# Kernel optimization log

Hardware: AMD Instinct MI355X
Metric: run time of the kernel (lower is better)

Reference implementation:

```python
import jax, jax.numpy as jnp
import numpy as np

B, N_EX, N_KC, D_E, D_C, D_H = 32, 1024, 128, 64, 64, 64


def setup_inputs() -> dict:
    key = jax.random.key(0)
    ks = jax.random.split(key, 20)
    return {
        "h": jax.random.normal(ks[0], (B, N_KC, D_H), jnp.float32),
        "ex": jax.random.uniform(ks[1], (B, N_EX), jnp.float32),
        "su": jax.random.uniform(ks[2], (B,), jnp.float32),
        "ex_graph": jax.random.uniform(ks[3], (N_EX, N_KC), jnp.float32),
        "kc_gamma": jax.random.normal(ks[4], (N_KC, N_KC), jnp.float32),
        "W_ex": jax.random.normal(ks[5], (D_E, 2 * N_EX), jnp.float32) * 0.02,
        "W_kc": jax.random.normal(ks[6], (D_C, N_KC), jnp.float32) * 0.05,
        "tgru_wih": jax.random.normal(ks[7], (3 * D_H, D_E), jnp.float32) * 0.05,
        "tgru_whh": jax.random.normal(ks[8], (3 * D_H, D_H), jnp.float32) * 0.05,
        "tgru_bih": jax.random.normal(ks[9], (3 * D_H,), jnp.float32) * 0.05,
        "tgru_bhh": jax.random.normal(ks[10], (3 * D_H,), jnp.float32) * 0.05,
        "fpart_w": jax.random.normal(ks[11], (D_H, D_C + D_H), jnp.float32) * 0.05,
        "fpart_b": jax.random.normal(ks[12], (D_H,), jnp.float32) * 0.05,
        "ulin_w": jax.random.normal(ks[13], (D_H, D_H), jnp.float32) * 0.05,
        "ulin_b": jax.random.normal(ks[14], (D_H,), jnp.float32) * 0.05,
        "ugru_wih": jax.random.normal(ks[15], (3 * D_H, D_H), jnp.float32) * 0.05,
        "ugru_whh": jax.random.normal(ks[16], (3 * D_H, D_H), jnp.float32) * 0.05,
        "ugru_bih": jax.random.normal(ks[17], (3 * D_H,), jnp.float32) * 0.05,
        "ugru_bhh": jax.random.normal(ks[18], (3 * D_H,), jnp.float32) * 0.05,
    }


def _gru_cell(x, h, wih, whh, bih, bhh):
    # torch.nn.GRUCell: gates in order r, z, n
    gi = x @ wih.T + bih
    gh = h @ whh.T + bhh
    ir, iz, inn = jnp.split(gi, 3, axis=-1)
    hr, hz, hn = jnp.split(gh, 3, axis=-1)
    r = jax.nn.sigmoid(ir + hr)
    z = jax.nn.sigmoid(iz + hz)
    n = jnp.tanh(inn + r * hn)
    return (1.0 - z) * n + z * h


def reference(h, ex, su, ex_graph, kc_gamma, W_ex, W_kc,
              tgru_wih, tgru_whh, tgru_bih, tgru_bhh,
              fpart_w, fpart_b, ulin_w, ulin_b,
              ugru_wih, ugru_whh, ugru_bih, ugru_bhh):
    bsz, n_kc, d_h = h.shape
    kc_graph = jax.nn.sigmoid(kc_gamma)  # (n_kc, n_kc)

    # exercise embedding from [ex*su, ex*(1-su)]
    x_id = jnp.concatenate([ex * su[:, None], ex * (1.0 - su)[:, None]], axis=-1)  # (B, 2*n_ex)
    x = x_id @ W_ex.T  # (B, d_e)

    kci = ex @ ex_graph  # (B, n_kc)
    kci_flat = kci.reshape(bsz * n_kc, 1)

    # temporal GRU update, gated by kci
    x_rep = jnp.broadcast_to(x[:, None, :], (bsz, n_kc, x.shape[-1])).reshape(bsz * n_kc, -1)
    h_flat = h.reshape(bsz * n_kc, d_h)
    th = _gru_cell(x_rep, h_flat, tgru_wih, tgru_whh, tgru_bih, tgru_bhh)
    new_h = (1.0 - kci_flat) * h_flat + kci_flat * th  # (B*n_kc, d_h)

    delta_h = (new_h - h_flat).reshape(bsz, n_kc, d_h)

    # kc_embeddings(eye(n_kc)) == W_kc.T : (n_kc, d_c)
    e = W_kc.T
    # fpart(concat([delta_h_i, e_j])) split into the two weight blocks
    W_dh = fpart_w[:, :d_h]   # acts on delta_h
    W_e = fpart_w[:, d_h:]    # acts on e
    dpart = delta_h @ W_dh.T                      # (B, n_kc_i, d_h)
    epart = e @ W_e.T + fpart_b                   # (n_kc_j, d_h)
    pre = dpart[:, :, None, :] + epart[None, None, :, :]  # (B, i, j, d_h)
    partij = jax.nn.relu(pre)
    partij = partij * kc_graph[None, :, :, None] * kci[:, :, None, None]
    partj = jnp.sum(partij, axis=1)               # (B, n_kc_j, d_h)

    outj = jax.nn.relu(partj @ ulin_w.T + ulin_b).reshape(bsz * n_kc, d_h)
    kcj = (kci @ kc_graph).reshape(bsz * n_kc, 1)

    uh = _gru_cell(outj, new_h, ugru_wih, ugru_whh, ugru_bih, ugru_bhh)
    h_out = (1.0 - kcj) * new_h + kcj * uh
    return h_out.reshape(bsz, n_kc, d_h)
```

## Files before the change

### kernel.cpp

```cpp
#include <hip/hip_runtime.h>
#include <math.h>

#define NB  32
#define NKC 128
#define DH  64
#define NEX 1024
#define G3  192

#define XOFF    0
#define KCIOFF  2048
#define KCGOFF  6144
#define EPOFF   22528
#define NHOFF   30720
#define DPOFF   292864

__device__ __forceinline__ float sigf(float x) { return 1.0f / (1.0f + expf(-x)); }

__global__ __launch_bounds__(256) void k1_prep(
    const float* __restrict__ ex, const float* __restrict__ su,
    const float* __restrict__ ex_graph, const float* __restrict__ kc_gamma,
    const float* __restrict__ W_ex, const float* __restrict__ W_kc,
    const float* __restrict__ fpart_w, const float* __restrict__ fpart_b,
    float* __restrict__ ws)
{
    int t = threadIdx.x, wave = t >> 6, lane = t & 63;
    int blk = blockIdx.x;
    __shared__ float kred[256];
    __shared__ float fwT[64 * 65];
    __shared__ float wkS[64 * 33];

    if (blk < 256) {
        int b = blk >> 3;
        int dbase = (blk & 7) * 8;
        float sub = su[b];
        const float* exb = ex + (size_t)b * NEX;
        float er[16];
        #pragma unroll
        for (int i = 0; i < 16; ++i) er[i] = exb[lane + i * 64];
        #pragma unroll
        for (int p = 0; p < 2; ++p) {
            int d = dbase + wave * 2 + p;
            const float* wr = W_ex + (size_t)d * (2 * NEX);
            float a1 = 0.f, a2 = 0.f;
            #pragma unroll
            for (int i = 0; i < 16; ++i) {
                int k = lane + i * 64;
                a1 = fmaf(er[i], wr[k], a1);
                a2 = fmaf(er[i], wr[NEX + k], a2);
            }
            float v = sub * a1 + (1.0f - sub) * a2;
            #pragma unroll
            for (int off = 32; off; off >>= 1) v += __shfl_down(v, off, 64);
            if (lane == 0) ws[XOFF + b * DH + d] = v;
        }
    } else if (blk < 384) {
        int q = blk - 256;
        int b = q >> 2, i0 = (q & 3) * 32;
        int i = t & 31, ks = t >> 5;
        const float* exb = ex + (size_t)b * NEX;
        const float* eg = ex_graph + i0 + i;
        int kb = ks * 128;
        float a = 0.f;
        for (int k = 0; k < 128; ++k)
            a = fmaf(exb[kb + k], eg[(size_t)(kb + k) * NKC], a);
        kred[t] = a;
        __syncthreads();
        if (t < 32) {
            float s = 0.f;
            #pragma unroll
            for (int r = 0; r < 8; ++r) s += kred[r * 32 + t];
            ws[KCIOFF + b * NKC + i0 + t] = s;
        }
    } else if (blk < 400) {
        int q = blk - 384;
        #pragma unroll
        for (int r = 0; r < 4; ++r) {
            int idx = q * 1024 + r * 256 + t;
            ws[KCGOFF + idx] = sigf(kc_gamma[idx]);
        }
    } else {
        int eb = blk - 400;
        for (int idx = t; idx < 4096; idx += 256) {
            int d = idx >> 6, c = idx & 63;
            fwT[c * 65 + d] = fpart_w[d * 128 + 64 + c];
        }
        for (int idx = t; idx < 2048; idx += 256) {
            int c = idx >> 5, jl = idx & 31;
            wkS[c * 33 + jl] = W_kc[(size_t)c * NKC + eb * 32 + jl];
        }
        __syncthreads();
        float fb = fpart_b[lane];
        #pragma unroll
        for (int q2 = 0; q2 < 8; ++q2) {
            int jl = wave + 4 * q2;
            float a = fb;
            for (int c = 0; c < 64; ++c)
                a = fmaf(wkS[c * 33 + jl], fwT[c * 65 + lane], a);
            ws[EPOFF + (eb * 32 + jl) * DH + lane] = a;
        }
    }
}

__global__ __launch_bounds__(256) void k2_tgru(
    const float* __restrict__ h, const float* __restrict__ tgru_wih,
    const float* __restrict__ tgru_whh, const float* __restrict__ tgru_bih,
    const float* __restrict__ tgru_bhh, const float* __restrict__ fpart_w,
    float* __restrict__ ws)
{
    int t = threadIdx.x, wave = t >> 6, lane = t & 63;
    int b = blockIdx.x >> 2;
    int i0 = (blockIdx.x & 3) * 32;
    __shared__ float whhT[32 * 193];
    __shared__ float wihT[32 * 193];
    __shared__ float ht[32 * DH];
    __shared__ float dlt[32 * DH];
    __shared__ float xs[DH];
    __shared__ float bih3[G3];
    __shared__ float bhh3[G3];
    __shared__ float kcis[32];

    const float* hb = h + (size_t)(b * NKC + i0) * DH;
    for (int idx = t; idx < 32 * DH; idx += 256) ht[idx] = hb[idx];
    if (t < DH) xs[t] = ws[XOFF + b * DH + t];
    if (t < G3) { bih3[t] = tgru_bih[t]; bhh3[t] = tgru_bhh[t]; }
    if (t < 32) kcis[t] = ws[KCIOFF + b * NKC + i0 + t];
    __syncthreads();

    float gir = bih3[lane], giz = bih3[64 + lane], gin = bih3[128 + lane];
    float ar[8], az[8], an[8];
    #pragma unroll
    for (int m = 0; m < 8; ++m) {
        ar[m] = bhh3[lane]; az[m] = bhh3[64 + lane]; an[m] = bhh3[128 + lane];
    }

    for (int ch = 0; ch < 2; ++ch) {
        __syncthreads();
        for (int idx = t; idx < G3 * 32; idx += 256) {
            int row = idx >> 5, kk = idx & 31;
            whhT[kk * 193 + row] = tgru_whh[row * DH + ch * 32 + kk];
            wihT[kk * 193 + row] = tgru_wih[row * DH + ch * 32 + kk];
        }
        __syncthreads();
        for (int kk = 0; kk < 32; ++kk) {
            float wr = whhT[kk * 193 + lane];
            float wz = whhT[kk * 193 + 64 + lane];
            float wn = whhT[kk * 193 + 128 + lane];
            float xk = xs[ch * 32 + kk];
            gir = fmaf(wihT[kk * 193 + lane], xk, gir);
            giz = fmaf(wihT[kk * 193 + 64 + lane], xk, giz);
            gin = fmaf(wihT[kk * 193 + 128 + lane], xk, gin);
            int k = ch * 32 + kk;
            #pragma unroll
            for (int m = 0; m < 8; ++m) {
                float hk = ht[(wave * 8 + m) * DH + k];
                ar[m] = fmaf(wr, hk, ar[m]);
                az[m] = fmaf(wz, hk, az[m]);
                an[m] = fmaf(wn, hk, an[m]);
            }
        }
    }
    #pragma unroll
    for (int m = 0; m < 8; ++m) {
        int il = wave * 8 + m;
        float hval = ht[il * DH + lane];
        float r = sigf(gir + ar[m]);
        float z = sigf(giz + az[m]);
        float n = tanhf(gin + r * an[m]);
        float th = (1.0f - z) * n + z * hval;
        float kv = kcis[il];
        float nh = (1.0f - kv) * hval + kv * th;
        ws[NHOFF + (size_t)(b * NKC + i0 + il) * DH + lane] = nh;
        dlt[il * DH + lane] = kv * (th - hval);
    }
    __syncthreads();
    for (int idx = t; idx < 4096; idx += 256) {
        int d = idx >> 6, k = idx & 63;
        whhT[k * 65 + d] = fpart_w[d * 128 + k];
    }
    __syncthreads();
    float acc[8];
    #pragma unroll
    for (int m = 0; m < 8; ++m) acc[m] = 0.f;
    for (int k = 0; k < 64; ++k) {
        float w = whhT[k * 65 + lane];
        #pragma unroll
        for (int m = 0; m < 8; ++m)
            acc[m] = fmaf(dlt[(wave * 8 + m) * DH + k], w, acc[m]);
    }
    #pragma unroll
    for (int m = 0; m < 8; ++m)
        ws[DPOFF + (size_t)(b * NKC + i0 + wave * 8 + m) * DH + lane] = acc[m];
}

__global__ __launch_bounds__(256) void k3_update(
    const float* __restrict__ ulin_w, const float* __restrict__ ulin_b,
    const float* __restrict__ ugru_wih, const float* __restrict__ ugru_whh,
    const float* __restrict__ ugru_bih, const float* __restrict__ ugru_bhh,
    float* __restrict__ ws, float* __restrict__ out)
{
    int t = threadIdx.x, wave = t >> 6, lane = t & 63;
    int b = blockIdx.x >> 3;
    int j0 = (blockIdx.x & 7) * 16;

    __shared__ float scratch[12352];
    __shared__ float pjS[16 * DH];
    __shared__ float outjS[16 * DH];
    __shared__ float newhS[16 * DH];
    __shared__ float kcis[NKC];
    __shared__ float kcjS[16];
    __shared__ float bihS[G3];
    __shared__ float bhhS[G3];

    float* dpartS = scratch;
    float* wjS    = scratch + 8192;
    float* epS    = scratch + 10240;

    const float* dp = ws + DPOFF + (size_t)b * NKC * DH;
    for (int idx = t; idx < NKC * DH; idx += 256) dpartS[idx] = dp[idx];
    if (t < NKC) kcis[t] = ws[KCIOFF + b * NKC + t];
    for (int idx = t; idx < 16 * DH; idx += 256) {
        epS[idx]   = ws[EPOFF + j0 * DH + idx];
        newhS[idx] = ws[NHOFF + (size_t)(b * NKC + j0) * DH + idx];
    }
    if (t < G3) { bihS[t] = ugru_bih[t]; bhhS[t] = ugru_bhh[t]; }
    __syncthreads();
    for (int idx = t; idx < 2048; idx += 256) {
        int i = idx >> 4, jl = idx & 15;
        wjS[idx] = kcis[i] * ws[KCGOFF + i * NKC + j0 + jl];
    }
    __syncthreads();
    if (t < 16) {
        float s = 0.f;
        for (int i = 0; i < NKC; ++i) s += wjS[i * 16 + t];
        kcjS[t] = s;
    }
    float ep[4], pa[4];
    #pragma unroll
    for (int q = 0; q < 4; ++q) { ep[q] = epS[(wave + 4 * q) * DH + lane]; pa[q] = 0.f; }
    for (int i = 0; i < NKC; ++i) {
        float dv = dpartS[i * DH + lane];
        #pragma unroll
        for (int q = 0; q < 4; ++q) {
            float pre = fmaxf(dv + ep[q], 0.f);
            pa[q] = fmaf(pre, wjS[i * 16 + wave + 4 * q], pa[q]);
        }
    }
    #pragma unroll
    for (int q = 0; q < 4; ++q) pjS[(wave + 4 * q) * DH + lane] = pa[q];
    __syncthreads();
    float* ulT = scratch;
    for (int idx = t; idx < 4096; idx += 256) {
        int d2 = idx >> 6, k = idx & 63;
        ulT[k * 65 + d2] = ulin_w[d2 * DH + k];
    }
    float ulb = ulin_b[lane];
    __syncthreads();
    #pragma unroll
    for (int q = 0; q < 4; ++q) {
        int jl = wave + 4 * q;
        float a = ulb;
        for (int k = 0; k < DH; ++k) a = fmaf(pjS[jl * DH + k], ulT[k * 65 + lane], a);
        outjS[jl * DH + lane] = fmaxf(a, 0.f);
    }
    float* wihT = scratch;
    float* whhT = scratch + 6176;
    float gir[4], giz[4], gin[4], ghr[4], ghz[4], ghn[4];
    #pragma unroll
    for (int q = 0; q < 4; ++q) { gir[q] = giz[q] = gin[q] = ghr[q] = ghz[q] = ghn[q] = 0.f; }
    for (int ch = 0; ch < 2; ++ch) {
        __syncthreads();
        for (int idx = t; idx < G3 * 32; idx += 256) {
            int row = idx >> 5, kk = idx & 31;
            wihT[kk * 193 + row] = ugru_wih[row * DH + ch * 32 + kk];
            whhT[kk * 193 + row] = ugru_whh[row * DH + ch * 32 + kk];
        }
        __syncthreads();
        for (int kk = 0; kk < 32; ++kk) {
            float wir = wihT[kk * 193 + lane];
            float wiz = wihT[kk * 193 + 64 + lane];
            float win = wihT[kk * 193 + 128 + lane];
            float wwr = whhT[kk * 193 + lane];
            float wwz = whhT[kk * 193 + 64 + lane];
            float wwn = whhT[kk * 193 + 128 + lane];
            int k = ch * 32 + kk;
            #pragma unroll
            for (int q = 0; q < 4; ++q) {
                int jl = wave + 4 * q;
                float ov = outjS[jl * DH + k];
                float nv = newhS[jl * DH + k];
                gir[q] = fmaf(wir, ov, gir[q]);
                giz[q] = fmaf(wiz, ov, giz[q]);
                gin[q] = fmaf(win, ov, gin[q]);
                ghr[q] = fmaf(wwr, nv, ghr[q]);
                ghz[q] = fmaf(wwz, nv, ghz[q]);
                ghn[q] = fmaf(wwn, nv, ghn[q]);
            }
        }
    }
    #pragma unroll
    for (int q = 0; q < 4; ++q) {
        int jl = wave + 4 * q;
        float r = sigf(gir[q] + bihS[lane] + ghr[q] + bhhS[lane]);
        float z = sigf(giz[q] + bihS[64 + lane] + ghz[q] + bhhS[64 + lane]);
        float n = tanhf(gin[q] + bihS[128 + lane] + r * (ghn[q] + bhhS[128 + lane]));
        float nh = newhS[jl * DH + lane];
        float uh = (1.0f - z) * n + z * nh;
        float kj = kcjS[jl];
        out[(size_t)(b * NKC + j0 + jl) * DH + lane] = (1.0f - kj) * nh + kj * uh;
    }
}

extern "C" void kernel_launch(void* const* d_in, const int* in_sizes, int n_in,
                              void* d_out, int out_size, void* d_ws, size_t ws_size,
                              hipStream_t stream) {
    const float* h        = (const float*)d_in[0];
    const float* ex       = (const float*)d_in[1];
    const float* su       = (const float*)d_in[2];
    const float* ex_graph = (const float*)d_in[3];
    const float* kc_gamma = (const float*)d_in[4];
    const float* W_ex     = (const float*)d_in[5];
    const float* W_kc     = (const float*)d_in[6];
    const float* tgru_wih = (const float*)d_in[7];
    const float* tgru_whh = (const float*)d_in[8];
    const float* tgru_bih = (const float*)d_in[9];
    const float* tgru_bhh = (const float*)d_in[10];
    const float* fpart_w  = (const float*)d_in[11];
    const float* fpart_b  = (const float*)d_in[12];
    const float* ulin_w   = (const float*)d_in[13];
    const float* ulin_b   = (const float*)d_in[14];
    const float* ugru_wih = (const float*)d_in[15];
    const float* ugru_whh = (const float*)d_in[16];
    const float* ugru_bih = (const float*)d_in[17];
    const float* ugru_bhh = (const float*)d_in[18];
    float* ws  = (float*)d_ws;
    float* out = (float*)d_out;

    hipLaunchKernelGGL(k1_prep, dim3(404), dim3(256), 0, stream,
                       ex, su, ex_graph, kc_gamma, W_ex, W_kc,
                       fpart_w, fpart_b, ws);
    hipLaunchKernelGGL(k2_tgru, dim3(128), dim3(256), 0, stream,
                       h, tgru_wih, tgru_whh, tgru_bih, tgru_bhh, fpart_w, ws);
    hipLaunchKernelGGL(k3_update, dim3(256), dim3(256), 0, stream,
                       ulin_w, ulin_b, ugru_wih, ugru_whh, ugru_bih, ugru_bhh,
                       ws, out);
}
```

Measured before the change: 150.2 us.

## Fuse prep kernel into GRU and update kernels, dropping one launch

Removes the separate prep kernel. The GRU kernel now computes the exercise projection x and kci itself from a shared-memory copy of ex, and its first four blocks also compute epart. The update kernel computes sigmoid(kc_gamma) inline instead of reading a precomputed table. This saves a kernel launch and the workspace round-trip, in exchange for redundant W_ex reads across the four blocks per batch (each now does all 64 dims) and longer serial work per block with only 128 blocks.

```diff
diff --git a/kernel.cpp b/kernel.cpp
--- a/kernel.cpp
+++ b/kernel.cpp
@@ -7,109 +7,27 @@
 #define NEX 1024
 #define G3  192
 
-#define XOFF    0
-#define KCIOFF  2048
-#define KCGOFF  6144
-#define EPOFF   22528
-#define NHOFF   30720
-#define DPOFF   292864
+#define KCIOFF  0
+#define EPOFF   4096
+#define NHOFF   12288
+#define DPOFF   274432
 
 __device__ __forceinline__ float sigf(float x) { return 1.0f / (1.0f + expf(-x)); }
 
-__global__ __launch_bounds__(256) void k1_prep(
-    const float* __restrict__ ex, const float* __restrict__ su,
-    const float* __restrict__ ex_graph, const float* __restrict__ kc_gamma,
+__global__ __launch_bounds__(256) void kA_tgru(
+    const float* __restrict__ h, const float* __restrict__ ex,
+    const float* __restrict__ su, const float* __restrict__ ex_graph,
     const float* __restrict__ W_ex, const float* __restrict__ W_kc,
+    const float* __restrict__ tgru_wih, const float* __restrict__ tgru_whh,
+    const float* __restrict__ tgru_bih, const float* __restrict__ tgru_bhh,
     const float* __restrict__ fpart_w, const float* __restrict__ fpart_b,
-    float* __restrict__ ws)
-{
-    int t = threadIdx.x, wave = t >> 6, lane = t & 63;
-    int blk = blockIdx.x;
-    __shared__ float kred[256];
-    __shared__ float fwT[64 * 65];
-    __shared__ float wkS[64 * 33];
-
-    if (blk < 256) {
-        int b = blk >> 3;
-        int dbase = (blk & 7) * 8;
-        float sub = su[b];
-        const float* exb = ex + (size_t)b * NEX;
-        float er[16];
-        #pragma unroll
-        for (int i = 0; i < 16; ++i) er[i] = exb[lane + i * 64];
-        #pragma unroll
-        for (int p = 0; p < 2; ++p) {
-            int d = dbase + wave * 2 + p;
-            const float* wr = W_ex + (size_t)d * (2 * NEX);
-            float a1 = 0.f, a2 = 0.f;
-            #pragma unroll
-            for (int i = 0; i < 16; ++i) {
-                int k = lane + i * 64;
-                a1 = fmaf(er[i], wr[k], a1);
-                a2 = fmaf(er[i], wr[NEX + k], a2);
-            }
-            float v = sub * a1 + (1.0f - sub) * a2;
-            #pragma unroll
-            for (int off = 32; off; off >>= 1) v += __shfl_down(v, off, 64);
-            if (lane == 0) ws[XOFF + b * DH + d] = v;
-        }
-    } else if (blk < 384) {
-        int q = blk - 256;
-        int b = q >> 2, i0 = (q & 3) * 32;
-        int i = t & 31, ks = t >> 5;
-        const float* exb = ex + (size_t)b * NEX;
-        const float* eg = ex_graph + i0 + i;
-        int kb = ks * 128;
-        float a = 0.f;
-        for (int k = 0; k < 128; ++k)
-            a = fmaf(exb[kb + k], eg[(size_t)(kb + k) * NKC], a);
-        kred[t] = a;
-        __syncthreads();
-        if (t < 32) {
-            float s = 0.f;
-            #pragma unroll
-            for (int r = 0; r < 8; ++r) s += kred[r * 32 + t];
-            ws[KCIOFF + b * NKC + i0 + t] = s;
-        }
-    } else if (blk < 400) {
-        int q = blk - 384;
-        #pragma unroll
-        for (int r = 0; r < 4; ++r) {
-            int idx = q * 1024 + r * 256 + t;
-            ws[KCGOFF + idx] = sigf(kc_gamma[idx]);
-        }
-    } else {
-        int eb = blk - 400;
-        for (int idx = t; idx < 4096; idx += 256) {
-            int d = idx >> 6, c = idx & 63;
-            fwT[c * 65 + d] = fpart_w[d * 128 + 64 + c];
-        }
-        for (int idx = t; idx < 2048; idx += 256) {
-            int c = idx >> 5, jl = idx & 31;
-            wkS[c * 33 + jl] = W_kc[(size_t)c * NKC + eb * 32 + jl];
-        }
-        __syncthreads();
-        float fb = fpart_b[lane];
-        #pragma unroll
-        for (int q2 = 0; q2 < 8; ++q2) {
-            int jl = wave + 4 * q2;
-            float a = fb;
-            for (int c = 0; c < 64; ++c)
-                a = fmaf(wkS[c * 33 + jl], fwT[c * 65 + lane], a);
-            ws[EPOFF + (eb * 32 + jl) * DH + lane] = a;
-        }
-    }
-}
-
-__global__ __launch_bounds__(256) void k2_tgru(
-    const float* __restrict__ h, const float* __restrict__ tgru_wih,
-    const float* __restrict__ tgru_whh, const float* __restrict__ tgru_bih,
-    const float* __restrict__ tgru_bhh, const float* __restrict__ fpart_w,
     float* __restrict__ ws)
 {
     int t = threadIdx.x, wave = t >> 6, lane = t & 63;
     int b = blockIdx.x >> 2;
     int i0 = (blockIdx.x & 3) * 32;
+
+    __shared__ float exs[NEX];
     __shared__ float whhT[32 * 193];
     __shared__ float wihT[32 * 193];
     __shared__ float ht[32 * DH];
@@ -117,14 +35,51 @@
     __shared__ float xs[DH];
     __shared__ float bih3[G3];
     __shared__ float bhh3[G3];
+    __shared__ float kred[256];
     __shared__ float kcis[32];
 
+    {
+        int idx = t * 4;
+        *(float4*)&exs[idx] = *(const float4*)&ex[(size_t)b * NEX + idx];
+    }
     const float* hb = h + (size_t)(b * NKC + i0) * DH;
     for (int idx = t; idx < 32 * DH; idx += 256) ht[idx] = hb[idx];
-    if (t < DH) xs[t] = ws[XOFF + b * DH + t];
     if (t < G3) { bih3[t] = tgru_bih[t]; bhh3[t] = tgru_bhh[t]; }
-    if (t < 32) kcis[t] = ws[KCIOFF + b * NKC + i0 + t];
-    __syncthreads();
+    __syncthreads();
+
+    float sub = su[b];
+    for (int m = 0; m < 16; ++m) {
+        int d = wave * 16 + m;
+        const float* wr = W_ex + (size_t)d * (2 * NEX);
+        float a1 = 0.f, a2 = 0.f;
+        #pragma unroll
+        for (int i = 0; i < 16; ++i) {
+            int k = lane + i * 64;
+            a1 = fmaf(exs[k], wr[k], a1);
+            a2 = fmaf(exs[k], wr[NEX + k], a2);
+        }
+        float v = sub * a1 + (1.0f - sub) * a2;
+        #pragma unroll
+        for (int off = 32; off; off >>= 1) v += __shfl_down(v, off, 64);
+        if (lane == 0) xs[d] = v;
+    }
+    {
+        int i = t & 31, ks = t >> 5;
+        const float* eg = ex_graph + i0 + i;
+        int kb = ks * 128;
+        float a = 0.f;
+        for (int k = 0; k < 128; ++k)
+            a = fmaf(exs[kb + k], eg[(size_t)(kb + k) * NKC], a);
+        kred[t] = a;
+    }
+    __syncthreads();
+    if (t < 32) {
+        float s = 0.f;
+        #pragma unroll
+        for (int r = 0; r < 8; ++r) s += kred[r * 32 + t];
+        kcis[t] = s;
+        ws[KCIOFF + b * NKC + i0 + t] = s;
+    }
 
     float gir = bih3[lane], giz = bih3[64 + lane], gin = bih3[128 + lane];
     float ar[8], az[8], an[8];
@@ -190,9 +145,35 @@
     #pragma unroll
     for (int m = 0; m < 8; ++m)
         ws[DPOFF + (size_t)(b * NKC + i0 + wave * 8 + m) * DH + lane] = acc[m];
+
+    if (blockIdx.x < 4) {
+        int eb = blockIdx.x;
+        __syncthreads();
+        float* fwT = whhT;
+        float* wkS = wihT;
+        for (int idx = t; idx < 4096; idx += 256) {
+            int d = idx >> 6, c = idx & 63;
+            fwT[c * 65 + d] = fpart_w[d * 128 + 64 + c];
+        }
+        for (int idx = t; idx < 2048; idx += 256) {
+            int c = idx >> 5, jl = idx & 31;
+            wkS[c * 33 + jl] = W_kc[(size_t)c * NKC + eb * 32 + jl];
+        }
+        __syncthreads();
+        float fb = fpart_b[lane];
+        #pragma unroll
+        for (int q2 = 0; q2 < 8; ++q2) {
+            int jl = wave + 4 * q2;
+            float a = fb;
+            for (int c = 0; c < 64; ++c)
+                a = fmaf(wkS[c * 33 + jl], fwT[c * 65 + lane], a);
+            ws[EPOFF + (eb * 32 + jl) * DH + lane] = a;
+        }
+    }
 }
 
-__global__ __launch_bounds__(256) void k3_update(
+__global__ __launch_bounds__(256) void kB_update(
+    const float* __restrict__ kc_gamma,
     const float* __restrict__ ulin_w, const float* __restrict__ ulin_b,
     const float* __restrict__ ugru_wih, const float* __restrict__ ugru_whh,
     const float* __restrict__ ugru_bih, const float* __restrict__ ugru_bhh,
@@ -226,7 +207,7 @@
     __syncthreads();
     for (int idx = t; idx < 2048; idx += 256) {
         int i = idx >> 4, jl = idx & 15;
-        wjS[idx] = kcis[i] * ws[KCGOFF + i * NKC + j0 + jl];
+        wjS[idx] = kcis[i] * sigf(kc_gamma[i * NKC + j0 + jl]);
     }
     __syncthreads();
     if (t < 16) {
@@ -335,12 +316,11 @@
     float* ws  = (float*)d_ws;
     float* out = (float*)d_out;
 
-    hipLaunchKernelGGL(k1_prep, dim3(404), dim3(256), 0, stream,
-                       ex, su, ex_graph, kc_gamma, W_ex, W_kc,
+    hipLaunchKernelGGL(kA_tgru, dim3(128), dim3(256), 0, stream,
+                       h, ex, su, ex_graph, W_ex, W_kc,
+                       tgru_wih, tgru_whh, tgru_bih, tgru_bhh,
                        fpart_w, fpart_b, ws);
-    hipLaunchKernelGGL(k2_tgru, dim3(128), dim3(256), 0, stream,
-                       h, tgru_wih, tgru_whh, tgru_bih, tgru_bhh, fpart_w, ws);
-    hipLaunchKernelGGL(k3_update, dim3(256), dim3(256), 0, stream,
-                       ulin_w, ulin_b, ugru_wih, ugru_whh, ugru_bih, ugru_bhh,
-                       ws, out);
+    hipLaunchKernelGGL(kB_update, dim3(256), dim3(256), 0, stream,
+                       kc_gamma, ulin_w, ulin_b,
+                       ugru_wih, ugru_whh, ugru_bih, ugru_bhh, ws, out);
 }
```

Result: slower. 159.0 us (+5.9%).

## Raise parallelism across kernels and fold kc_graph sigmoid into update kernel

Applied to the files above, without the earlier changes.

Splits the kci reduction into more, smaller blocks and doubles the tgru kernel's grid with 16 rows per block. Both GRU-style kernels move to 512-thread blocks so each wave handles fewer rows. The input-gate matvec in tgru is computed once by 192 threads instead of redundantly by every wave. The sigmoid of kc_gamma is now computed on the fly in the update kernel, which removes a workspace buffer and a prep branch. The aim is better GPU occupancy across the CUs, at the cost of less weight reuse per block and more per-block shared-memory staging.

```diff
diff --git a/kernel.cpp b/kernel.cpp
--- a/kernel.cpp
+++ b/kernel.cpp
@@ -9,19 +9,17 @@
 
 #define XOFF    0
 #define KCIOFF  2048
-#define KCGOFF  6144
-#define EPOFF   22528
-#define NHOFF   30720
-#define DPOFF   292864
+#define EPOFF   6144
+#define NHOFF   14336
+#define DPOFF   276480
 
 __device__ __forceinline__ float sigf(float x) { return 1.0f / (1.0f + expf(-x)); }
 
-__global__ __launch_bounds__(256) void k1_prep(
+__global__ __launch_bounds__(256) void k0_prep(
     const float* __restrict__ ex, const float* __restrict__ su,
-    const float* __restrict__ ex_graph, const float* __restrict__ kc_gamma,
-    const float* __restrict__ W_ex, const float* __restrict__ W_kc,
-    const float* __restrict__ fpart_w, const float* __restrict__ fpart_b,
-    float* __restrict__ ws)
+    const float* __restrict__ ex_graph, const float* __restrict__ W_ex,
+    const float* __restrict__ W_kc, const float* __restrict__ fpart_w,
+    const float* __restrict__ fpart_b, float* __restrict__ ws)
 {
     int t = threadIdx.x, wave = t >> 6, lane = t & 63;
     int blk = blockIdx.x;
@@ -53,33 +51,27 @@
             for (int off = 32; off; off >>= 1) v += __shfl_down(v, off, 64);
             if (lane == 0) ws[XOFF + b * DH + d] = v;
         }
-    } else if (blk < 384) {
+    } else if (blk < 512) {
         int q = blk - 256;
-        int b = q >> 2, i0 = (q & 3) * 32;
-        int i = t & 31, ks = t >> 5;
+        int b = q >> 3, i0 = (q & 7) * 16;
+        int i = t & 15, ks = t >> 4;
         const float* exb = ex + (size_t)b * NEX;
         const float* eg = ex_graph + i0 + i;
-        int kb = ks * 128;
+        int kb = ks * 64;
         float a = 0.f;
-        for (int k = 0; k < 128; ++k)
+        #pragma unroll 4
+        for (int k = 0; k < 64; ++k)
             a = fmaf(exb[kb + k], eg[(size_t)(kb + k) * NKC], a);
         kred[t] = a;
         __syncthreads();
-        if (t < 32) {
+        if (t < 16) {
             float s = 0.f;
             #pragma unroll
-            for (int r = 0; r < 8; ++r) s += kred[r * 32 + t];
+            for (int r = 0; r < 16; ++r) s += kred[r * 16 + t];
             ws[KCIOFF + b * NKC + i0 + t] = s;
         }
-    } else if (blk < 400) {
-        int q = blk - 384;
-        #pragma unroll
-        for (int r = 0; r < 4; ++r) {
-            int idx = q * 1024 + r * 256 + t;
-            ws[KCGOFF + idx] = sigf(kc_gamma[idx]);
-        }
     } else {
-        int eb = blk - 400;
+        int eb = blk - 512;
         for (int idx = t; idx < 4096; idx += 256) {
             int d = idx >> 6, c = idx & 63;
             fwT[c * 65 + d] = fpart_w[d * 128 + 64 + c];
@@ -101,71 +93,74 @@
     }
 }
 
-__global__ __launch_bounds__(256) void k2_tgru(
+__global__ __launch_bounds__(512) void k1_tgru(
     const float* __restrict__ h, const float* __restrict__ tgru_wih,
     const float* __restrict__ tgru_whh, const float* __restrict__ tgru_bih,
     const float* __restrict__ tgru_bhh, const float* __restrict__ fpart_w,
     float* __restrict__ ws)
 {
     int t = threadIdx.x, wave = t >> 6, lane = t & 63;
-    int b = blockIdx.x >> 2;
-    int i0 = (blockIdx.x & 3) * 32;
+    int b = blockIdx.x >> 3;
+    int i0 = (blockIdx.x & 7) * 16;
+
     __shared__ float whhT[32 * 193];
     __shared__ float wihT[32 * 193];
-    __shared__ float ht[32 * DH];
-    __shared__ float dlt[32 * DH];
+    __shared__ float ht[16 * DH];
+    __shared__ float dlt[16 * DH];
     __shared__ float xs[DH];
-    __shared__ float bih3[G3];
+    __shared__ float gis[G3];
     __shared__ float bhh3[G3];
-    __shared__ float kcis[32];
+    __shared__ float kcis[16];
 
     const float* hb = h + (size_t)(b * NKC + i0) * DH;
-    for (int idx = t; idx < 32 * DH; idx += 256) ht[idx] = hb[idx];
+    for (int idx = t; idx < 16 * DH; idx += 512) ht[idx] = hb[idx];
     if (t < DH) xs[t] = ws[XOFF + b * DH + t];
-    if (t < G3) { bih3[t] = tgru_bih[t]; bhh3[t] = tgru_bhh[t]; }
-    if (t < 32) kcis[t] = ws[KCIOFF + b * NKC + i0 + t];
-    __syncthreads();
-
-    float gir = bih3[lane], giz = bih3[64 + lane], gin = bih3[128 + lane];
-    float ar[8], az[8], an[8];
-    #pragma unroll
-    for (int m = 0; m < 8; ++m) {
+    if (t < G3) bhh3[t] = tgru_bhh[t];
+    if (t < 16) kcis[t] = ws[KCIOFF + b * NKC + i0 + t];
+    __syncthreads();
+
+    float giA = (t < G3) ? tgru_bih[t] : 0.f;
+    float ar[2], az[2], an[2];
+    #pragma unroll
+    for (int m = 0; m < 2; ++m) {
         ar[m] = bhh3[lane]; az[m] = bhh3[64 + lane]; an[m] = bhh3[128 + lane];
     }
 
     for (int ch = 0; ch < 2; ++ch) {
         __syncthreads();
-        for (int idx = t; idx < G3 * 32; idx += 256) {
+        for (int idx = t; idx < G3 * 32; idx += 512) {
             int row = idx >> 5, kk = idx & 31;
             whhT[kk * 193 + row] = tgru_whh[row * DH + ch * 32 + kk];
             wihT[kk * 193 + row] = tgru_wih[row * DH + ch * 32 + kk];
         }
         __syncthreads();
+        if (t < G3) {
+            for (int kk = 0; kk < 32; ++kk)
+                giA = fmaf(wihT[kk * 193 + t], xs[ch * 32 + kk], giA);
+        }
         for (int kk = 0; kk < 32; ++kk) {
             float wr = whhT[kk * 193 + lane];
             float wz = whhT[kk * 193 + 64 + lane];
             float wn = whhT[kk * 193 + 128 + lane];
-            float xk = xs[ch * 32 + kk];
-            gir = fmaf(wihT[kk * 193 + lane], xk, gir);
-            giz = fmaf(wihT[kk * 193 + 64 + lane], xk, giz);
-            gin = fmaf(wihT[kk * 193 + 128 + lane], xk, gin);
             int k = ch * 32 + kk;
             #pragma unroll
-            for (int m = 0; m < 8; ++m) {
-                float hk = ht[(wave * 8 + m) * DH + k];
+            for (int m = 0; m < 2; ++m) {
+                float hk = ht[(wave * 2 + m) * DH + k];
                 ar[m] = fmaf(wr, hk, ar[m]);
                 az[m] = fmaf(wz, hk, az[m]);
                 an[m] = fmaf(wn, hk, an[m]);
             }
         }
     }
-    #pragma unroll
-    for (int m = 0; m < 8; ++m) {
-        int il = wave * 8 + m;
+    if (t < G3) gis[t] = giA;
+    __syncthreads();
+    #pragma unroll
+    for (int m = 0; m < 2; ++m) {
+        int il = wave * 2 + m;
         float hval = ht[il * DH + lane];
-        float r = sigf(gir + ar[m]);
-        float z = sigf(giz + az[m]);
-        float n = tanhf(gin + r * an[m]);
+        float r = sigf(gis[lane] + ar[m]);
+        float z = sigf(gis[64 + lane] + az[m]);
+        float n = tanhf(gis[128 + lane] + r * an[m]);
         float th = (1.0f - z) * n + z * hval;
         float kv = kcis[il];
         float nh = (1.0f - kv) * hval + kv * th;
@@ -173,26 +168,26 @@
         dlt[il * DH + lane] = kv * (th - hval);
     }
     __syncthreads();
-    for (int idx = t; idx < 4096; idx += 256) {
+    for (int idx = t; idx < 4096; idx += 512) {
         int d = idx >> 6, k = idx & 63;
         whhT[k * 65 + d] = fpart_w[d * 128 + k];
     }
     __syncthreads();
-    float acc[8];
-    #pragma unroll
-    for (int m = 0; m < 8; ++m) acc[m] = 0.f;
+    float acc[2];
+    acc[0] = 0.f; acc[1] = 0.f;
     for (int k = 0; k < 64; ++k) {
         float w = whhT[k * 65 + lane];
         #pragma unroll
-        for (int m = 0; m < 8; ++m)
-            acc[m] = fmaf(dlt[(wave * 8 + m) * DH + k], w, acc[m]);
-    }
-    #pragma unroll
-    for (int m = 0; m < 8; ++m)
-        ws[DPOFF + (size_t)(b * NKC + i0 + wave * 8 + m) * DH + lane] = acc[m];
+        for (int m = 0; m < 2; ++m)
+            acc[m] = fmaf(dlt[(wave * 2 + m) * DH + k], w, acc[m]);
+    }
+    #pragma unroll
+    for (int m = 0; m < 2; ++m)
+        ws[DPOFF + (size_t)(b * NKC + i0 + wave * 2 + m) * DH + lane] = acc[m];
 }
 
-__global__ __launch_bounds__(256) void k3_update(
+__global__ __launch_bounds__(512) void kB_update(
+    const float* __restrict__ kc_gamma,
     const float* __restrict__ ulin_w, const float* __restrict__ ulin_b,
     const float* __restrict__ ugru_wih, const float* __restrict__ ugru_whh,
     const float* __restrict__ ugru_bih, const float* __restrict__ ugru_bhh,
@@ -216,17 +211,17 @@
     float* epS    = scratch + 10240;
 
     const float* dp = ws + DPOFF + (size_t)b * NKC * DH;
-    for (int idx = t; idx < NKC * DH; idx += 256) dpartS[idx] = dp[idx];
+    for (int idx = t; idx < NKC * DH; idx += 512) dpartS[idx] = dp[idx];
     if (t < NKC) kcis[t] = ws[KCIOFF + b * NKC + t];
-    for (int idx = t; idx < 16 * DH; idx += 256) {
+    for (int idx = t; idx < 16 * DH; idx += 512) {
         epS[idx]   = ws[EPOFF + j0 * DH + idx];
         newhS[idx] = ws[NHOFF + (size_t)(b * NKC + j0) * DH + idx];
     }
     if (t < G3) { bihS[t] = ugru_bih[t]; bhhS[t] = ugru_bhh[t]; }
     __syncthreads();
-    for (int idx = t; idx < 2048; idx += 256) {
+    for (int idx = t; idx < 2048; idx += 512) {
         int i = idx >> 4, jl = idx & 15;
-        wjS[idx] = kcis[i] * ws[KCGOFF + i * NKC + j0 + jl];
+        wjS[idx] = kcis[i] * sigf(kc_gamma[i * NKC + j0 + jl]);
     }
     __syncthreads();
     if (t < 16) {
@@ -234,42 +229,42 @@
         for (int i = 0; i < NKC; ++i) s += wjS[i * 16 + t];
         kcjS[t] = s;
     }
-    float ep[4], pa[4];
-    #pragma unroll
-    for (int q = 0; q < 4; ++q) { ep[q] = epS[(wave + 4 * q) * DH + lane]; pa[q] = 0.f; }
+    float ep[2], pa[2];
+    #pragma unroll
+    for (int m = 0; m < 2; ++m) { ep[m] = epS[(wave * 2 + m) * DH + lane]; pa[m] = 0.f; }
     for (int i = 0; i < NKC; ++i) {
         float dv = dpartS[i * DH + lane];
         #pragma unroll
-        for (int q = 0; q < 4; ++q) {
-            float pre = fmaxf(dv + ep[q], 0.f);
-            pa[q] = fmaf(pre, wjS[i * 16 + wave + 4 * q], pa[q]);
-        }
-    }
-    #pragma unroll
-    for (int q = 0; q < 4; ++q) pjS[(wave + 4 * q) * DH + lane] = pa[q];
+        for (int m = 0; m < 2; ++m) {
+            float pre = fmaxf(dv + ep[m], 0.f);
+            pa[m] = fmaf(pre, wjS[i * 16 + wave * 2 + m], pa[m]);
+        }
+    }
+    #pragma unroll
+    for (int m = 0; m < 2; ++m) pjS[(wave * 2 + m) * DH + lane] = pa[m];
     __syncthreads();
     float* ulT = scratch;
-    for (int idx = t; idx < 4096; idx += 256) {
+    for (int idx = t; idx < 4096; idx += 512) {
         int d2 = idx >> 6, k = idx & 63;
         ulT[k * 65 + d2] = ulin_w[d2 * DH + k];
     }
     float ulb = ulin_b[lane];
     __syncthreads();
     #pragma unroll
-    for (int q = 0; q < 4; ++q) {
-        int jl = wave + 4 * q;
+    for (int m = 0; m < 2; ++m) {
+        int jl = wave * 2 + m;
         float a = ulb;
         for (int k = 0; k < DH; ++k) a = fmaf(pjS[jl * DH + k], ulT[k * 65 + lane], a);
         outjS[jl * DH + lane] = fmaxf(a, 0.f);
     }
     float* wihT = scratch;
     float* whhT = scratch + 6176;
-    float gir[4], giz[4], gin[4], ghr[4], ghz[4], ghn[4];
-    #pragma unroll
-    for (int q = 0; q < 4; ++q) { gir[q] = giz[q] = gin[q] = ghr[q] = ghz[q] = ghn[q] = 0.f; }
+    float gir[2], giz[2], gin[2], ghr[2], ghz[2], ghn[2];
+    #pragma unroll
+    for (int m = 0; m < 2; ++m) { gir[m] = giz[m] = gin[m] = ghr[m] = ghz[m] = ghn[m] = 0.f; }
     for (int ch = 0; ch < 2; ++ch) {
         __syncthreads();
-        for (int idx = t; idx < G3 * 32; idx += 256) {
+        for (int idx = t; idx < G3 * 32; idx += 512) {
             int row = idx >> 5, kk = idx & 31;
             wihT[kk * 193 + row] = ugru_wih[row * DH + ch * 32 + kk];
             whhT[kk * 193 + row] = ugru_whh[row * DH + ch * 32 + kk];
@@ -284,25 +279,25 @@
             float wwn = whhT[kk * 193 + 128 + lane];
             int k = ch * 32 + kk;
             #pragma unroll
-            for (int q = 0; q < 4; ++q) {
-                int jl = wave + 4 * q;
+            for (int m = 0; m < 2; ++m) {
+                int jl = wave * 2 + m;
                 float ov = outjS[jl * DH + k];
                 float nv = newhS[jl * DH + k];
-                gir[q] = fmaf(wir, ov, gir[q]);
-                giz[q] = fmaf(wiz, ov, giz[q]);
-                gin[q] = fmaf(win, ov, gin[q]);
-                ghr[q] = fmaf(wwr, nv, ghr[q]);
-                ghz[q] = fmaf(wwz, nv, ghz[q]);
-                ghn[q] = fmaf(wwn, nv, ghn[q]);
+                gir[m] = fmaf(wir, ov, gir[m]);
+                giz[m] = fmaf(wiz, ov, giz[m]);
+                gin[m] = fmaf(win, ov, gin[m]);
+                ghr[m] = fmaf(wwr, nv, ghr[m]);
+                ghz[m] = fmaf(wwz, nv, ghz[m]);
+                ghn[m] = fmaf(wwn, nv, ghn[m]);
             }
         }
     }
     #pragma unroll
-    for (int q = 0; q < 4; ++q) {
-        int jl = wave + 4 * q;
-        float r = sigf(gir[q] + bihS[lane] + ghr[q] + bhhS[lane]);
-        float z = sigf(giz[q] + bihS[64 + lane] + ghz[q] + bhhS[64 + lane]);
-        float n = tanhf(gin[q] + bihS[128 + lane] + r * (ghn[q] + bhhS[128 + lane]));
+    for (int m = 0; m < 2; ++m) {
+        int jl = wave * 2 + m;
+        float r = sigf(gir[m] + bihS[lane] + ghr[m] + bhhS[lane]);
+        float z = sigf(giz[m] + bihS[64 + lane] + ghz[m] + bhhS[64 + lane]);
+        float n = tanhf(gin[m] + bihS[128 + lane] + r * (ghn[m] + bhhS[128 + lane]));
         float nh = newhS[jl * DH + lane];
         float uh = (1.0f - z) * n + z * nh;
         float kj = kcjS[jl];
@@ -335,12 +330,11 @@
     float* ws  = (float*)d_ws;
     float* out = (float*)d_out;
 
-    hipLaunchKernelGGL(k1_prep, dim3(404), dim3(256), 0, stream,
-                       ex, su, ex_graph, kc_gamma, W_ex, W_kc,
-                       fpart_w, fpart_b, ws);
-    hipLaunchKernelGGL(k2_tgru, dim3(128), dim3(256), 0, stream,
+    hipLaunchKernelGGL(k0_prep, dim3(516), dim3(256), 0, stream,
+                       ex, su, ex_graph, W_ex, W_kc, fpart_w, fpart_b, ws);
+    hipLaunchKernelGGL(k1_tgru, dim3(256), dim3(512), 0, stream,
                        h, tgru_wih, tgru_whh, tgru_bih, tgru_bhh, fpart_w, ws);
-    hipLaunchKernelGGL(k3_update, dim3(256), dim3(256), 0, stream,
-                       ulin_w, ulin_b, ugru_wih, ugru_whh, ugru_bih, ugru_bhh,
-                       ws, out);
+    hipLaunchKernelGGL(kB_update, dim3(256), dim3(512), 0, stream,
+                       kc_gamma, ulin_w, ulin_b,
+                       ugru_wih, ugru_whh, ugru_bih, ugru_bhh, ws, out);
 }
```

Result: no change. 150.4 us (+0.1%).
